# Optimization experiments

Hardware: AMD Instinct MI355X
Metric: run time of the kernel (lower is better)

## Reference

```python
import jax, jax.numpy as jnp
import numpy as np

NUM_HEADS = 16


def setup_inputs() -> dict:
    key = jax.random.key(0)
    ks = jax.random.split(key, 7)
    B, S, D = 2, 2048, 1024
    return {
        "query": jax.random.normal(ks[0], (B, S, D), jnp.float32),
        "key": jax.random.normal(ks[1], (B, S, D), jnp.float32),
        "value": jax.random.normal(ks[2], (B, S, D), jnp.float32),
        "qk_w": jax.random.normal(ks[3], (2 * D, D), jnp.float32) * (D ** -0.5),
        "qk_b": jax.random.normal(ks[4], (2 * D,), jnp.float32) * 0.02,
        "out_w": jax.random.normal(ks[5], (D, D), jnp.float32) * (D ** -0.5),
        "out_b": jax.random.normal(ks[6], (D,), jnp.float32) * 0.02,
    }


def reference(query, key, value, qk_w, qk_b, out_w, out_b):
    # Hand-rolled multi-head attention with fused QK projection (both Q and K
    # come from `query`); `key` arg is unused (as in the source forward).
    B, S, D = query.shape
    H = NUM_HEADS
    dh = D // H
    scale = D ** -0.5  # source uses d_model**-0.5, not head_dim

    qk = query @ qk_w.T + qk_b                      # [B, S, 2D]
    qk = qk.reshape(B, S, 2, H, dh).transpose(2, 0, 3, 1, 4)  # [2, B, H, S, dh]
    q, k = qk[0], qk[1]                              # [B, H, S, dh]

    scores = jnp.einsum("bhqd,bhkd->bhqk", q, k) * scale  # [B, H, S, S]
    attn = jax.nn.softmax(scores, axis=-1)
    # dropout_p = 0.0 -> identity (eval mode)

    v = value.reshape(B, S, H, dh).transpose(0, 2, 1, 3)   # [B, H, S, dh]
    out = jnp.einsum("bhqk,bhkd->bhqd", attn, v)           # [B, H, S, dh]
    out = out.transpose(0, 2, 1, 3).reshape(B, S, D)       # merge heads
    return out @ out_w.T + out_b
```

## Files before the change

### kernel.cpp

```cpp
#include <hip/hip_runtime.h>
#include <hip/hip_bf16.h>
#include <stdint.h>

typedef __attribute__((ext_vector_type(8))) short bf16x8;
typedef __attribute__((ext_vector_type(4))) short bf16x4;
typedef __attribute__((ext_vector_type(4))) float f32x4;
typedef __attribute__((ext_vector_type(16))) float f32x16;

#define B_ 2
#define H_ 16
#define S_ 2048
#define D_ 1024
#define DH 64

__device__ __forceinline__ void gload_lds16(const void* g, void* l) {
  __builtin_amdgcn_global_load_lds((const __attribute__((address_space(1))) void*)g,
                                   (__attribute__((address_space(3))) void*)l, 16, 0, 0);
}

__device__ __forceinline__ float exp2_hw(float x) {
  float r;
  asm("v_exp_f32 %0, %1" : "=v"(r) : "v"(x));
  return r;
}

__device__ __forceinline__ uint32_t packbf2(float lo, float hi) {
  union { __hip_bfloat162 h; uint32_t u; } u;
  u.h = __float22bfloat162_rn(make_float2(lo, hi));
  return u.u;
}

__device__ __forceinline__ void pl32swap(uint32_t& a, uint32_t& b) {
  asm volatile("v_permlane32_swap_b32 %0, %1" : "+v"(a), "+v"(b));
}

__global__ void k_f2b3(const float* __restrict__ a, __hip_bfloat16* __restrict__ da,
                       const float* __restrict__ b, __hip_bfloat16* __restrict__ db,
                       const float* __restrict__ c, __hip_bfloat16* __restrict__ dc) {
  int i = blockIdx.x * blockDim.x + threadIdx.x;
  const float* src;
  __hip_bfloat16* dst;
  int off;
  if (i < 524288) { src = a; dst = da; off = i; }
  else if (i < 786432) { src = b; dst = db; off = i - 524288; }
  else { src = c; dst = dc; off = i - 786432; }
  const float4* p = (const float4*)src + (size_t)off * 2;
  float4 x = p[0], y = p[1];
  union { bf16x8 v; __hip_bfloat16 h[8]; } u;
  u.h[0] = __float2bfloat16(x.x); u.h[1] = __float2bfloat16(x.y);
  u.h[2] = __float2bfloat16(x.z); u.h[3] = __float2bfloat16(x.w);
  u.h[4] = __float2bfloat16(y.x); u.h[5] = __float2bfloat16(y.y);
  u.h[6] = __float2bfloat16(y.z); u.h[7] = __float2bfloat16(y.w);
  *((bf16x8*)dst + off) = u.v;
}

__global__ void k_vt(const float* __restrict__ v, __hip_bfloat16* __restrict__ vt) {
  __shared__ float tile[64][65];
  const int bh = blockIdx.y, b = bh >> 4, h = bh & 15;
  const int s0 = blockIdx.x * 64;
  const int t = threadIdx.x;
#pragma unroll
  for (int it = 0; it < 4; ++it) {
    const int r = it * 16 + (t >> 4);
    const int c = (t & 15) * 4;
    const float4 x = *(const float4*)(v + (size_t)(b * S_ + s0 + r) * D_ + h * DH + c);
    tile[r][c] = x.x; tile[r][c + 1] = x.y; tile[r][c + 2] = x.z; tile[r][c + 3] = x.w;
  }
  __syncthreads();
#pragma unroll
  for (int it = 0; it < 4; ++it) {
    const int d = it * 16 + (t >> 4);
    const int j = (t & 15) * 4;
    union { bf16x4 v4; __hip_bfloat16 e[4]; } u;
    u.e[0] = __float2bfloat16(tile[j][d]);
    u.e[1] = __float2bfloat16(tile[j + 1][d]);
    u.e[2] = __float2bfloat16(tile[j + 2][d]);
    u.e[3] = __float2bfloat16(tile[j + 3][d]);
    *(bf16x4*)(vt + (size_t)(bh * DH + d) * S_ + s0 + j) = u.v4;
  }
}

__device__ __forceinline__ void gemm_core(
    const __hip_bfloat16* __restrict__ A, const __hip_bfloat16* __restrict__ Bm,
    int m0, int n0, __hip_bfloat16* As, __hip_bfloat16* Bs, f32x4 acc[4][4]) {
  const int t = threadIdx.x;
  const int l = t & 63, w = t >> 6;
  const int wr = w >> 1, wc = w & 1;
  const int lr = l & 15, lc = l >> 4;
  const int slot = (t & 7) ^ ((t >> 3) & 7);
  const int r0 = t >> 3;
  const __hip_bfloat16* gA = A + (size_t)(m0 + r0) * 1024 + slot * 8;
  const __hip_bfloat16* gB = Bm + (size_t)(n0 + r0) * 1024 + slot * 8;
  char* AsB = (char*)As;
  char* BsB = (char*)Bs;

#define GSTAGE(bi, k0)                                               \
  {                                                                  \
    char* la = AsB + (bi) * 16384 + t * 16;                          \
    char* lb = BsB + (bi) * 16384 + t * 16;                          \
    _Pragma("unroll") for (int c = 0; c < 4; ++c) {                  \
      gload_lds16(gA + (size_t)(c * 32) * 1024 + (k0), la + c * 4096); \
      gload_lds16(gB + (size_t)(c * 32) * 1024 + (k0), lb + c * 4096); \
    }                                                                \
  }

  GSTAGE(0, 0)
  __syncthreads();
  int buf = 0;
  for (int it = 0; it < 16; ++it) {
    if (it < 15) GSTAGE(buf ^ 1, (it + 1) * 64)
    const char* ab = AsB + buf * 16384;
    const char* bb = BsB + buf * 16384;
#pragma unroll
    for (int kk = 0; kk < 2; ++kk) {
      bf16x8 af[4], bv[4];
#pragma unroll
      for (int i = 0; i < 4; ++i) {
        const int r = wr * 64 + i * 16 + lr;
        af[i] = *(const bf16x8*)(ab + r * 128 + (((kk * 4 + lc) ^ (r & 7)) << 4));
      }
#pragma unroll
      for (int j = 0; j < 4; ++j) {
        const int r = wc * 64 + j * 16 + lr;
        bv[j] = *(const bf16x8*)(bb + r * 128 + (((kk * 4 + lc) ^ (r & 7)) << 4));
      }
#pragma unroll
      for (int i = 0; i < 4; ++i)
#pragma unroll
        for (int j = 0; j < 4; ++j)
          acc[i][j] = __builtin_amdgcn_mfma_f32_16x16x32_bf16(af[i], bv[j], acc[i][j], 0, 0, 0);
    }
    __syncthreads();
    buf ^= 1;
  }
#undef GSTAGE
}

__global__ __launch_bounds__(256) void k_gemm_qk(
    const __hip_bfloat16* __restrict__ A, const __hip_bfloat16* __restrict__ Bm,
    const float* __restrict__ bias,
    __hip_bfloat16* __restrict__ Qh, __hip_bfloat16* __restrict__ Kh) {
  __shared__ __align__(16) __hip_bfloat16 As[2][128 * 64];
  __shared__ __align__(16) __hip_bfloat16 Bs[2][128 * 64];
  f32x4 acc[4][4] = {};
  const int m0 = blockIdx.x * 128, n0 = blockIdx.y * 128;
  gemm_core(A, Bm, m0, n0, &As[0][0], &Bs[0][0], acc);
  const int t = threadIdx.x, l = t & 63, w = t >> 6;
  const int wr = w >> 1, wc = w & 1, lr = l & 15, lc = l >> 4;
#pragma unroll
  for (int j = 0; j < 4; ++j) {
    const int col = n0 + wc * 64 + j * 16 + lr;
    const float bv = bias[col];
    const int inK = col >> 10;
    const int hh = (col & 1023) >> 6, dd = col & 63;
    __hip_bfloat16* dst = inK ? Kh : Qh;
    const float sc = inK ? 1.0f : 0.045084220f;
#pragma unroll
    for (int i = 0; i < 4; ++i) {
#pragma unroll
      for (int r = 0; r < 4; ++r) {
        const int row = m0 + wr * 64 + i * 16 + lc * 4 + r;
        const int b = row >> 11, s = row & 2047;
        const float vv = (acc[i][j][r] + bv) * sc;
        dst[((size_t)(b * H_ + hh) * S_ + s) * DH + dd] = __float2bfloat16(vv);
      }
    }
  }
}

__global__ __launch_bounds__(256) void k_gemm_out(
    const __hip_bfloat16* __restrict__ A, const __hip_bfloat16* __restrict__ Bm,
    const float* __restrict__ bias, float* __restrict__ out) {
  __shared__ __align__(16) __hip_bfloat16 As[2][128 * 64];
  __shared__ __align__(16) __hip_bfloat16 Bs[2][128 * 64];
  f32x4 acc[4][4] = {};
  const int m0 = blockIdx.x * 128, n0 = blockIdx.y * 128;
  gemm_core(A, Bm, m0, n0, &As[0][0], &Bs[0][0], acc);
  const int t = threadIdx.x, l = t & 63, w = t >> 6;
  const int wr = w >> 1, wc = w & 1, lr = l & 15, lc = l >> 4;
#pragma unroll
  for (int j = 0; j < 4; ++j) {
    const int col = n0 + wc * 64 + j * 16 + lr;
    const float bv = bias[col];
#pragma unroll
    for (int i = 0; i < 4; ++i) {
#pragma unroll
      for (int r = 0; r < 4; ++r) {
        const int row = m0 + wr * 64 + i * 16 + lc * 4 + r;
        out[(size_t)row * D_ + col] = acc[i][j][r] + bv;
      }
    }
  }
}

__global__ __launch_bounds__(256, 4) void k_attn(
    const __hip_bfloat16* __restrict__ Qh, const __hip_bfloat16* __restrict__ Kh,
    const __hip_bfloat16* __restrict__ VT,
    __hip_bfloat16* __restrict__ pO0, __hip_bfloat16* __restrict__ pO1,
    float* __restrict__ l0a, float* __restrict__ l1a) {
  __shared__ __align__(16) __hip_bfloat16 KV[2][8192];
  const int bh = blockIdx.y, q0 = blockIdx.x * 128;
  const int half = blockIdx.z;
  const int jbeg = half << 10, jend = jbeg + 1024;
  const int t = threadIdx.x, l = t & 63, w = t >> 6;
  const int qi = l & 31, hi = l >> 5;
  const __hip_bfloat16* Qb = Qh + (size_t)bh * S_ * DH;
  const __hip_bfloat16* Kb = Kh + (size_t)bh * S_ * DH;
  const __hip_bfloat16* Vb = VT + (size_t)bh * DH * S_;

  bf16x8 qf[4];
#pragma unroll
  for (int dc = 0; dc < 4; ++dc)
    qf[dc] = *(const bf16x8*)&Qb[(size_t)(q0 + w * 32 + qi) * DH + dc * 16 + hi * 8];

  const int tr = t >> 4, tc = t & 15;
  const int c0 = tc ^ (tr & 15);
  const int c1 = tc ^ ((tr + 16) & 15);
  const __hip_bfloat16* gK0 = Kb + (size_t)(tr + (c0 >= 8 ? 32 : 0)) * DH + (c0 & 7) * 8;
  const __hip_bfloat16* gK1 = Kb + (size_t)(tr + 16 + (c1 >= 8 ? 32 : 0)) * DH + (c1 & 7) * 8;
  const __hip_bfloat16* gV0 = Vb + (size_t)(tr + (c0 >= 8 ? 32 : 0)) * S_ + (c0 & 7) * 8;
  const __hip_bfloat16* gV1 = Vb + (size_t)(tr + 16 + (c1 >= 8 ? 32 : 0)) * S_ + (c1 & 7) * 8;

#define STAGE(bufi, j0)                                              \
  {                                                                  \
    __hip_bfloat16* Ld = &KV[bufi][0];                               \
    gload_lds16(gK0 + (size_t)(j0) * DH, Ld + t * 8);                \
    gload_lds16(gK1 + (size_t)(j0) * DH, Ld + 2048 + t * 8);         \
    gload_lds16(gV0 + (j0), Ld + 4096 + t * 8);                      \
    gload_lds16(gV1 + (j0), Ld + 4096 + 2048 + t * 8);               \
  }

  f32x16 oacc0 = {}, oacc1 = {};
  float lsum = 0.f;
  int buf = 0;

  STAGE(0, jbeg)
  __syncthreads();

  const int rsw = (qi & 15) << 4;

  for (int j0 = jbeg; j0 < jend; j0 += 64) {
    if (j0 + 64 < jend) STAGE(buf ^ 1, j0 + 64)
    const char* KsB = (const char*)&KV[buf][0];
    const char* VsB = (const char*)&KV[buf][4096];

    f32x16 s0 = {}, s1 = {};
    __builtin_amdgcn_s_setprio(1);
#pragma unroll
    for (int dc = 0; dc < 4; ++dc) {
      const int cb = dc * 32 + hi * 16;
      const bf16x8 kf0 = *(const bf16x8*)(KsB + qi * 256 + (cb ^ rsw));
      const bf16x8 kf1 = *(const bf16x8*)(KsB + qi * 256 + ((128 + cb) ^ rsw));
      s0 = __builtin_amdgcn_mfma_f32_32x32x16_bf16(kf0, qf[dc], s0, 0, 0, 0);
      s1 = __builtin_amdgcn_mfma_f32_32x32x16_bf16(kf1, qf[dc], s1, 0, 0, 0);
    }
    __builtin_amdgcn_s_setprio(0);

#pragma unroll
    for (int r = 0; r < 16; ++r) s0[r] = exp2_hw(s0[r]);
#pragma unroll
    for (int r = 0; r < 16; ++r) s1[r] = exp2_hw(s1[r]);
    float ts[16];
#pragma unroll
    for (int r = 0; r < 16; ++r) ts[r] = s0[r] + s1[r];
#pragma unroll
    for (int st = 8; st > 0; st >>= 1)
#pragma unroll
      for (int r = 0; r < st; ++r) ts[r] += ts[r + st];
    lsum += ts[0] + __shfl_xor(ts[0], 32, 64);

#define PVSTEP(SS, KSOFF)                                                         \
  {                                                                               \
    uint32_t w0 = packbf2(SS[0], SS[1]), w1 = packbf2(SS[2], SS[3]);              \
    uint32_t w2 = packbf2(SS[4], SS[5]), w3 = packbf2(SS[6], SS[7]);              \
    uint32_t w4 = packbf2(SS[8], SS[9]), w5 = packbf2(SS[10], SS[11]);            \
    uint32_t w6 = packbf2(SS[12], SS[13]), w7 = packbf2(SS[14], SS[15]);          \
    pl32swap(w0, w2); pl32swap(w1, w3); pl32swap(w4, w6); pl32swap(w5, w7);       \
    union { bf16x8 v; uint32_t u[4]; } pa0, pa1;                                  \
    pa0.u[0] = w0; pa0.u[1] = w1; pa0.u[2] = w2; pa0.u[3] = w3;                   \
    pa1.u[0] = w4; pa1.u[1] = w5; pa1.u[2] = w6; pa1.u[3] = w7;                   \
    const int cb = (KSOFF) + hi * 16;                                             \
    bf16x8 vf;                                                                    \
    vf = *(const bf16x8*)(VsB + qi * 256 + ((cb + 0) ^ rsw));                     \
    oacc0 = __builtin_amdgcn_mfma_f32_32x32x16_bf16(pa0.v, vf, oacc0, 0, 0, 0);   \
    vf = *(const bf16x8*)(VsB + qi * 256 + ((cb + 32) ^ rsw));                    \
    oacc0 = __builtin_amdgcn_mfma_f32_32x32x16_bf16(pa1.v, vf, oacc0, 0, 0, 0);   \
    vf = *(const bf16x8*)(VsB + qi * 256 + ((cb + 128) ^ rsw));                   \
    oacc1 = __builtin_amdgcn_mfma_f32_32x32x16_bf16(pa0.v, vf, oacc1, 0, 0, 0);   \
    vf = *(const bf16x8*)(VsB + qi * 256 + ((cb + 128 + 32) ^ rsw));              \
    oacc1 = __builtin_amdgcn_mfma_f32_32x32x16_bf16(pa1.v, vf, oacc1, 0, 0, 0);   \
  }
    __builtin_amdgcn_s_setprio(1);
    PVSTEP(s0, 0)
    PVSTEP(s1, 64)
    __builtin_amdgcn_s_setprio(0);

    __syncthreads();
    buf ^= 1;
  }

  __hip_bfloat16* pO = half ? pO1 : pO0;
  float* la = half ? l1a : l0a;
  const size_t rowb = (size_t)bh * S_ + q0 + w * 32;
#pragma unroll
  for (int r = 0; r < 16; ++r) {
    const int qloc = (r & 3) + 8 * (r >> 2) + 4 * hi;
    pO[(rowb + qloc) * 64 + qi] = __float2bfloat16(oacc0[r]);
    pO[(rowb + qloc) * 64 + 32 + qi] = __float2bfloat16(oacc1[r]);
  }
  if (l < 32) la[rowb + qi] = lsum;
#undef STAGE
#undef PVSTEP
}

__global__ __launch_bounds__(256) void k_combine(
    const __hip_bfloat16* __restrict__ pO0, const __hip_bfloat16* __restrict__ pO1,
    const float* __restrict__ l0a, const float* __restrict__ l1a,
    __hip_bfloat16* __restrict__ aO) {
  const int tid = blockIdx.x * 256 + threadIdx.x;
  const float inv = 1.0f / (l0a[tid] + l1a[tid]);
  const bf16x8* r0 = (const bf16x8*)(pO0 + (size_t)tid * 64);
  const bf16x8* r1 = (const bf16x8*)(pO1 + (size_t)tid * 64);
  const int bh = tid >> 11, s = tid & 2047, bb = bh >> 4, h = bh & 15;
  __hip_bfloat16* o = aO + ((size_t)(bb * S_ + s)) * D_ + h * DH;
#pragma unroll
  for (int j = 0; j < 8; ++j) {
    union { bf16x8 v; __hip_bfloat16 e[8]; } v0, v1, u;
    v0.v = r0[j]; v1.v = r1[j];
#pragma unroll
    for (int e = 0; e < 8; ++e)
      u.e[e] = __float2bfloat16(inv * (__bfloat162float(v0.e[e]) + __bfloat162float(v1.e[e])));
    *(bf16x8*)(o + j * 8) = u.v;
  }
}

extern "C" void kernel_launch(void* const* d_in, const int* in_sizes, int n_in,
                              void* d_out, int out_size, void* d_ws, size_t ws_size,
                              hipStream_t stream) {
  const float* q   = (const float*)d_in[0];
  const float* val = (const float*)d_in[2];
  const float* qkw = (const float*)d_in[3];
  const float* qkb = (const float*)d_in[4];
  const float* ow  = (const float*)d_in[5];
  const float* ob  = (const float*)d_in[6];
  float* out = (float*)d_out;

  __hip_bfloat16* ws  = (__hip_bfloat16*)d_ws;
  __hip_bfloat16* qA  = ws;
  __hip_bfloat16* w1b = qA + 4194304;
  __hip_bfloat16* w2b = w1b + 2097152;
  __hip_bfloat16* Qh  = w2b + 1048576;
  __hip_bfloat16* Kh  = Qh + 4194304;
  __hip_bfloat16* VT  = Kh + 4194304;
  __hip_bfloat16* aO  = VT + 4194304;
  __hip_bfloat16* pO1 = aO + 4194304;
  __hip_bfloat16* pO0 = qA;
  float* l0a = (float*)w1b;
  float* l1a = l0a + 65536;

  hipLaunchKernelGGL(k_f2b3, dim3(3584), dim3(256), 0, stream, q, qA, qkw, w1b, ow, w2b);
  hipLaunchKernelGGL(k_vt, dim3(32, 32), dim3(256), 0, stream, val, VT);
  hipLaunchKernelGGL(k_gemm_qk, dim3(32, 16), dim3(256), 0, stream, qA, w1b, qkb, Qh, Kh);
  hipLaunchKernelGGL(k_attn, dim3(16, 32, 2), dim3(256), 0, stream, Qh, Kh, VT, pO0, pO1, l0a, l1a);
  hipLaunchKernelGGL(k_combine, dim3(256), dim3(256), 0, stream, pO0, pO1, l0a, l1a, aO);
  hipLaunchKernelGGL(k_gemm_out, dim3(32, 8), dim3(256), 0, stream, aO, w2b, ob, out);
}
```

Measured before the change: 121.6 us.

## Split attention KV into four chunks, MFMA row sums, XCD-aware GEMM tile mapping

```diff
diff --git a/kernel.cpp b/kernel.cpp
--- a/kernel.cpp
+++ b/kernel.cpp
@@ -143,7 +143,11 @@
   __shared__ __align__(16) __hip_bfloat16 As[2][128 * 64];
   __shared__ __align__(16) __hip_bfloat16 Bs[2][128 * 64];
   f32x4 acc[4][4] = {};
-  const int m0 = blockIdx.x * 128, n0 = blockIdx.y * 128;
+  const int orig = blockIdx.x + blockIdx.y * 32;
+  const int xcd = orig & 7, idx = orig >> 3;
+  const int mb = (xcd & 3) * 8 + (idx & 7);
+  const int nb = (xcd >> 2) * 8 + (idx >> 3);
+  const int m0 = mb * 128, n0 = nb * 128;
   gemm_core(A, Bm, m0, n0, &As[0][0], &Bs[0][0], acc);
   const int t = threadIdx.x, l = t & 63, w = t >> 6;
   const int wr = w >> 1, wc = w & 1, lr = l & 15, lc = l >> 4;
@@ -174,7 +178,11 @@
   __shared__ __align__(16) __hip_bfloat16 As[2][128 * 64];
   __shared__ __align__(16) __hip_bfloat16 Bs[2][128 * 64];
   f32x4 acc[4][4] = {};
-  const int m0 = blockIdx.x * 128, n0 = blockIdx.y * 128;
+  const int orig = blockIdx.x + blockIdx.y * 32;
+  const int xcd = orig & 7, idx = orig >> 3;
+  const int mb = (xcd & 3) * 8 + (idx & 7);
+  const int nb = (xcd >> 2) * 4 + (idx >> 3);
+  const int m0 = mb * 128, n0 = nb * 128;
   gemm_core(A, Bm, m0, n0, &As[0][0], &Bs[0][0], acc);
   const int t = threadIdx.x, l = t & 63, w = t >> 6;
   const int wr = w >> 1, wc = w & 1, lr = l & 15, lc = l >> 4;
@@ -197,11 +205,13 @@
     const __hip_bfloat16* __restrict__ Qh, const __hip_bfloat16* __restrict__ Kh,
     const __hip_bfloat16* __restrict__ VT,
     __hip_bfloat16* __restrict__ pO0, __hip_bfloat16* __restrict__ pO1,
-    float* __restrict__ l0a, float* __restrict__ l1a) {
+    __hip_bfloat16* __restrict__ pO2, __hip_bfloat16* __restrict__ pO3,
+    float* __restrict__ l0a, float* __restrict__ l1a,
+    float* __restrict__ l2a, float* __restrict__ l3a, int jlen) {
   __shared__ __align__(16) __hip_bfloat16 KV[2][8192];
   const int bh = blockIdx.y, q0 = blockIdx.x * 128;
-  const int half = blockIdx.z;
-  const int jbeg = half << 10, jend = jbeg + 1024;
+  const int z = blockIdx.z;
+  const int jbeg = z * jlen, jend = jbeg + jlen;
   const int t = threadIdx.x, l = t & 63, w = t >> 6;
   const int qi = l & 31, hi = l >> 5;
   const __hip_bfloat16* Qb = Qh + (size_t)bh * S_ * DH;
@@ -212,6 +222,10 @@
 #pragma unroll
   for (int dc = 0; dc < 4; ++dc)
     qf[dc] = *(const bf16x8*)&Qb[(size_t)(q0 + w * 32 + qi) * DH + dc * 16 + hi * 8];
+
+  union { bf16x8 v; short e[8]; } one8;
+#pragma unroll
+  for (int i = 0; i < 8; ++i) one8.e[i] = (short)0x3F80;
 
   const int tr = t >> 4, tc = t & 15;
   const int c0 = tc ^ (tr & 15);
@@ -230,8 +244,7 @@
     gload_lds16(gV1 + (j0), Ld + 4096 + 2048 + t * 8);               \
   }
 
-  f32x16 oacc0 = {}, oacc1 = {};
-  float lsum = 0.f;
+  f32x16 oacc0 = {}, oacc1 = {}, lacc = {};
   int buf = 0;
 
   STAGE(0, jbeg)
@@ -260,14 +273,6 @@
     for (int r = 0; r < 16; ++r) s0[r] = exp2_hw(s0[r]);
 #pragma unroll
     for (int r = 0; r < 16; ++r) s1[r] = exp2_hw(s1[r]);
-    float ts[16];
-#pragma unroll
-    for (int r = 0; r < 16; ++r) ts[r] = s0[r] + s1[r];
-#pragma unroll
-    for (int st = 8; st > 0; st >>= 1)
-#pragma unroll
-      for (int r = 0; r < st; ++r) ts[r] += ts[r + st];
-    lsum += ts[0] + __shfl_xor(ts[0], 32, 64);
 
 #define PVSTEP(SS, KSOFF)                                                         \
   {                                                                               \
@@ -289,6 +294,8 @@
     oacc1 = __builtin_amdgcn_mfma_f32_32x32x16_bf16(pa0.v, vf, oacc1, 0, 0, 0);   \
     vf = *(const bf16x8*)(VsB + qi * 256 + ((cb + 128 + 32) ^ rsw));              \
     oacc1 = __builtin_amdgcn_mfma_f32_32x32x16_bf16(pa1.v, vf, oacc1, 0, 0, 0);   \
+    lacc = __builtin_amdgcn_mfma_f32_32x32x16_bf16(pa0.v, one8.v, lacc, 0, 0, 0); \
+    lacc = __builtin_amdgcn_mfma_f32_32x32x16_bf16(pa1.v, one8.v, lacc, 0, 0, 0); \
   }
     __builtin_amdgcn_s_setprio(1);
     PVSTEP(s0, 0)
@@ -299,8 +306,8 @@
     buf ^= 1;
   }
 
-  __hip_bfloat16* pO = half ? pO1 : pO0;
-  float* la = half ? l1a : l0a;
+  __hip_bfloat16* pO = z == 0 ? pO0 : z == 1 ? pO1 : z == 2 ? pO2 : pO3;
+  float* la = z == 0 ? l0a : z == 1 ? l1a : z == 2 ? l2a : l3a;
   const size_t rowb = (size_t)bh * S_ + q0 + w * 32;
 #pragma unroll
   for (int r = 0; r < 16; ++r) {
@@ -308,28 +315,49 @@
     pO[(rowb + qloc) * 64 + qi] = __float2bfloat16(oacc0[r]);
     pO[(rowb + qloc) * 64 + 32 + qi] = __float2bfloat16(oacc1[r]);
   }
-  if (l < 32) la[rowb + qi] = lsum;
+  if (qi == 0) {
+#pragma unroll
+    for (int r = 0; r < 16; ++r) {
+      const int qloc = (r & 3) + 8 * (r >> 2) + 4 * hi;
+      la[rowb + qloc] = lacc[r];
+    }
+  }
 #undef STAGE
 #undef PVSTEP
 }
 
 __global__ __launch_bounds__(256) void k_combine(
     const __hip_bfloat16* __restrict__ pO0, const __hip_bfloat16* __restrict__ pO1,
+    const __hip_bfloat16* __restrict__ pO2, const __hip_bfloat16* __restrict__ pO3,
     const float* __restrict__ l0a, const float* __restrict__ l1a,
-    __hip_bfloat16* __restrict__ aO) {
+    const float* __restrict__ l2a, const float* __restrict__ l3a,
+    __hip_bfloat16* __restrict__ aO, int ns) {
   const int tid = blockIdx.x * 256 + threadIdx.x;
-  const float inv = 1.0f / (l0a[tid] + l1a[tid]);
+  float lt = l0a[tid] + l1a[tid];
+  if (ns == 4) lt += l2a[tid] + l3a[tid];
+  const float inv = 1.0f / lt;
   const bf16x8* r0 = (const bf16x8*)(pO0 + (size_t)tid * 64);
   const bf16x8* r1 = (const bf16x8*)(pO1 + (size_t)tid * 64);
+  const bf16x8* r2 = (const bf16x8*)(pO2 + (size_t)tid * 64);
+  const bf16x8* r3 = (const bf16x8*)(pO3 + (size_t)tid * 64);
   const int bh = tid >> 11, s = tid & 2047, bb = bh >> 4, h = bh & 15;
   __hip_bfloat16* o = aO + ((size_t)(bb * S_ + s)) * D_ + h * DH;
 #pragma unroll
   for (int j = 0; j < 8; ++j) {
-    union { bf16x8 v; __hip_bfloat16 e[8]; } v0, v1, u;
+    union { bf16x8 v; __hip_bfloat16 e[8]; } v0, v1, v2, v3, u;
     v0.v = r0[j]; v1.v = r1[j];
+    float acc[8];
 #pragma unroll
     for (int e = 0; e < 8; ++e)
-      u.e[e] = __float2bfloat16(inv * (__bfloat162float(v0.e[e]) + __bfloat162float(v1.e[e])));
+      acc[e] = __bfloat162float(v0.e[e]) + __bfloat162float(v1.e[e]);
+    if (ns == 4) {
+      v2.v = r2[j]; v3.v = r3[j];
+#pragma unroll
+      for (int e = 0; e < 8; ++e)
+        acc[e] += __bfloat162float(v2.e[e]) + __bfloat162float(v3.e[e]);
+    }
+#pragma unroll
+    for (int e = 0; e < 8; ++e) u.e[e] = __float2bfloat16(acc[e] * inv);
     *(bf16x8*)(o + j * 8) = u.v;
   }
 }
@@ -353,15 +381,25 @@
   __hip_bfloat16* Kh  = Qh + 4194304;
   __hip_bfloat16* VT  = Kh + 4194304;
   __hip_bfloat16* aO  = VT + 4194304;
-  __hip_bfloat16* pO1 = aO + 4194304;
-  __hip_bfloat16* pO0 = qA;
+  __hip_bfloat16* pOt = aO + 4194304;
+
+  const bool four = ws_size >= 81788928ull;
+  const int nsplit = four ? 4 : 2;
+  __hip_bfloat16* pO0 = four ? pOt : qA;
+  __hip_bfloat16* pO1 = four ? pOt + 4194304 : pOt;
+  __hip_bfloat16* pO2 = four ? pOt + 8388608 : pOt;
+  __hip_bfloat16* pO3 = four ? pOt + 12582912 : pOt;
   float* l0a = (float*)w1b;
   float* l1a = l0a + 65536;
+  float* l2a = l1a + 65536;
+  float* l3a = l2a + 65536;
 
   hipLaunchKernelGGL(k_f2b3, dim3(3584), dim3(256), 0, stream, q, qA, qkw, w1b, ow, w2b);
   hipLaunchKernelGGL(k_vt, dim3(32, 32), dim3(256), 0, stream, val, VT);
   hipLaunchKernelGGL(k_gemm_qk, dim3(32, 16), dim3(256), 0, stream, qA, w1b, qkb, Qh, Kh);
-  hipLaunchKernelGGL(k_attn, dim3(16, 32, 2), dim3(256), 0, stream, Qh, Kh, VT, pO0, pO1, l0a, l1a);
-  hipLaunchKernelGGL(k_combine, dim3(256), dim3(256), 0, stream, pO0, pO1, l0a, l1a, aO);
+  hipLaunchKernelGGL(k_attn, dim3(16, 32, nsplit), dim3(256), 0, stream, Qh, Kh, VT,
+                     pO0, pO1, pO2, pO3, l0a, l1a, l2a, l3a, S_ / nsplit);
+  hipLaunchKernelGGL(k_combine, dim3(256), dim3(256), 0, stream,
+                     pO0, pO1, pO2, pO3, l0a, l1a, l2a, l3a, aO, nsplit);
   hipLaunchKernelGGL(k_gemm_out, dim3(32, 8), dim3(256), 0, stream, aO, w2b, ob, out);
 }
```

Result: slower. 165.7 us (+36.2%).
